# Kernel tuning notes

Measured on AMD Instinct MI355X. Metric: run time of the kernel, lower is better.

Reference implementation:

```python
import jax, jax.numpy as jnp
import numpy as np

EPS = 1e-6

def setup_inputs() -> dict:
    key = jax.random.key(0)
    k1, k2, k3 = jax.random.split(key, 3)
    N, L, S, H, D = 8, 4096, 4096, 8, 64
    queries = jax.random.normal(k1, (N, L, H, D), dtype=jnp.float32)
    keys = jax.random.normal(k2, (N, S, H, D), dtype=jnp.float32)
    values = jax.random.normal(k3, (N, S, H, D), dtype=jnp.float32)
    return {"queries": queries, "keys": keys, "values": values}

def reference(queries, keys, values):
    # elu(x)+1 feature maps (positive kernel)
    Q = jax.nn.elu(queries) + 1.0  # [N,L,H,D]
    K = jax.nn.elu(keys) + 1.0     # [N,S,H,D]
    v_length = values.shape[1]
    v = values / v_length          # scale for numerical stability
    # per-head KV state: [N,H,D,Dv]
    KV = jnp.einsum('nshd,nshv->nhdv', K, v)
    # normalizer: [N,L,H]
    K_sum = K.sum(axis=1)  # [N,H,D]
    Z = 1.0 / (jnp.einsum('nlhd,nhd->nlh', Q, K_sum) + EPS)
    out = jnp.einsum('nlhd,nhdv,nlh->nlhv', Q, KV, Z) * v_length
    return out
```

## Files before the change

### kernel.cpp

```cpp
#include <hip/hip_runtime.h>
#include <hip/hip_bf16.h>
#include <cstddef>
#include <cstdint>

#define N_B   8
#define L_L   4096
#define S_S   4096
#define H_H   8
#define D_D   64
#define NH    64
#define KVLD  68
#define KVSZ  (65 * KVLD)

typedef const float __attribute__((address_space(1)))* gas_fp;
typedef float __attribute__((address_space(3)))* las_fp;

__device__ __forceinline__ float elu1(float x) {
    return x > 0.f ? x + 1.f : __expf(x);
}

__global__ __launch_bounds__(256, 3)
void la_phase1(const float* __restrict__ Kin, const float* __restrict__ Vin,
               float* __restrict__ partials, int split, int schunk)
{
    __shared__ union {
        struct { float K[64 * 64]; float V[2][64 * 64]; } st;
        float acc[64 * 68];
    } sm;
    __shared__ float sKsumP[4 * 64];

    const int b     = blockIdx.x;
    const int nh    = b / split;
    const int chunk = b - nh * split;
    const int n     = nh >> 3;
    const int h     = nh & 7;
    const int s0    = chunk * schunk;

    const int tid  = threadIdx.x;
    const int w    = tid >> 6;
    const int lane = tid & 63;
    const int dg   = lane >> 3;
    const int vg   = lane & 7;

    float acc[8][8];
    #pragma unroll
    for (int i = 0; i < 8; ++i)
        #pragma unroll
        for (int j = 0; j < 8; ++j) acc[i][j] = 0.f;
    float ksum = 0.f;

    const int kd = lane;

    const int lrow = lane >> 4;
    const int lcol = (lane & 15) * 4;

    const float* Kb = Kin + (size_t)n * S_S * (H_H * D_D) + h * D_D;
    const float* Vb = Vin + (size_t)n * S_S * (H_H * D_D) + h * D_D;

    const int ntiles = schunk >> 6;

    #pragma unroll
    for (int c = 0; c < 4; ++c) {
        const int r = w * 16 + c * 4 + lrow;
        __builtin_amdgcn_global_load_lds(
            (gas_fp)(Vb + (size_t)(s0 + r) * (H_H * D_D) + lcol),
            (las_fp)&sm.st.V[0][(w * 16 + c * 4) * 64], 16, 0, 0);
    }

    for (int t = 0; t < ntiles; ++t) {
        const int srow = s0 + t * 64;

        #pragma unroll
        for (int c = 0; c < 4; ++c) {
            const int r = w * 16 + c * 4 + lrow;
            float4 kv = *(const float4*)(Kb + (size_t)(srow + r) * (H_H * D_D) + lcol);
            kv.x = elu1(kv.x); kv.y = elu1(kv.y);
            kv.z = elu1(kv.z); kv.w = elu1(kv.w);
            *(float4*)&sm.st.K[(w * 16 + c * 4) * 64 + lane * 4] = kv;
        }

        if (t + 1 < ntiles) {
            const int srn = srow + 64;
            #pragma unroll
            for (int c = 0; c < 4; ++c) {
                const int r = w * 16 + c * 4 + lrow;
                __builtin_amdgcn_global_load_lds(
                    (gas_fp)(Vb + (size_t)(srn + r) * (H_H * D_D) + lcol),
                    (las_fp)&sm.st.V[(t & 1) ^ 1][(w * 16 + c * 4) * 64], 16, 0, 0);
            }
            asm volatile("s_waitcnt vmcnt(4)" ::: "memory");
        } else {
            asm volatile("s_waitcnt vmcnt(0)" ::: "memory");
        }

        const float* Kbuf = sm.st.K;
        const float* Vbuf = sm.st.V[t & 1];

        #pragma unroll 4
        for (int sl = 0; sl < 16; ++sl) {
            const int s = w * 16 + sl;
            const float4 k0 = *(const float4*)&Kbuf[s * 64 + dg * 8];
            const float4 k1 = *(const float4*)&Kbuf[s * 64 + dg * 8 + 4];
            const float4 v0 = *(const float4*)&Vbuf[s * 64 + vg * 8];
            const float4 v1 = *(const float4*)&Vbuf[s * 64 + vg * 8 + 4];
            const float kf[8] = {k0.x, k0.y, k0.z, k0.w, k1.x, k1.y, k1.z, k1.w};
            const float vf[8] = {v0.x, v0.y, v0.z, v0.w, v1.x, v1.y, v1.z, v1.w};
            #pragma unroll
            for (int i = 0; i < 8; ++i)
                #pragma unroll
                for (int j = 0; j < 8; ++j)
                    acc[i][j] = fmaf(kf[i], vf[j], acc[i][j]);
        }
        #pragma unroll
        for (int sl = 0; sl < 16; ++sl)
            ksum += Kbuf[(w * 16 + sl) * 64 + kd];
    }
    __syncthreads();

    for (int ww = 0; ww < 4; ++ww) {
        if (w == ww) {
            #pragma unroll
            for (int i = 0; i < 8; ++i) {
                float* p = &sm.acc[(dg * 8 + i) * 68 + vg * 8];
                if (ww == 0) {
                    *(float4*)p       = make_float4(acc[i][0], acc[i][1], acc[i][2], acc[i][3]);
                    *(float4*)(p + 4) = make_float4(acc[i][4], acc[i][5], acc[i][6], acc[i][7]);
                } else {
                    float4 a0 = *(const float4*)p;
                    float4 a1 = *(const float4*)(p + 4);
                    a0.x += acc[i][0]; a0.y += acc[i][1]; a0.z += acc[i][2]; a0.w += acc[i][3];
                    a1.x += acc[i][4]; a1.y += acc[i][5]; a1.z += acc[i][6]; a1.w += acc[i][7];
                    *(float4*)p       = a0;
                    *(float4*)(p + 4) = a1;
                }
            }
        }
        __syncthreads();
    }

    sKsumP[w * 64 + kd] = ksum;
    __syncthreads();

    float* outp = partials + (size_t)b * KVSZ;
    for (int idx = tid; idx < KVSZ; idx += 256) {
        const int r = idx / KVLD;
        const int c = idx - r * KVLD;
        float val = 0.f;
        if (c < 64) {
            if (r < 64)
                val = sm.acc[idx];
            else
                val = sKsumP[c] + sKsumP[64 + c] + sKsumP[128 + c] + sKsumP[192 + c];
        }
        outp[idx] = val;
    }
}

__global__ __launch_bounds__(256)
void la_reduce(const float* __restrict__ partials, float* __restrict__ kvt, int split)
{
    const int idx = blockIdx.x * 256 + threadIdx.x;
    if (idx >= NH * KVSZ) return;
    const int nh  = idx / KVSZ;
    const int rem = idx - nh * KVSZ;
    const float* p = partials + (size_t)nh * split * KVSZ + rem;
    float s = 0.f;
    for (int c = 0; c < split; ++c) s += p[(size_t)c * KVSZ];
    kvt[idx] = s;
}

__global__ __launch_bounds__(256, 2)
void la_phase2(const float* __restrict__ Qin, const float* __restrict__ kvt,
               float* __restrict__ Out)
{
    __shared__ float sQ[128 * 68];
    __shared__ float sKV[KVSZ];

    const int b   = blockIdx.x;
    const int nh  = b >> 5;
    const int lc  = b & 31;
    const int n   = nh >> 3;
    const int h   = nh & 7;
    const int tid = threadIdx.x;
    const int w    = tid >> 6;
    const int lane = tid & 63;

    const float* Qc = Qin + (((size_t)n * L_L + (size_t)lc * 128) * H_H + h) * D_D;
    float*       Oc = Out + (((size_t)n * L_L + (size_t)lc * 128) * H_H + h) * D_D;

    {
        const float4* src = (const float4*)(kvt + (size_t)nh * KVSZ);
        float4*       dst = (float4*)sKV;
        #pragma unroll
        for (int it = 0; it < 4; ++it)
            dst[it * 256 + tid] = src[it * 256 + tid];
        if (tid < 81) dst[1024 + tid] = src[1024 + tid];
    }

    #pragma unroll
    for (int it = 0; it < 8; ++it) {
        const int slot = it * 256 + tid;
        const int r    = slot >> 4;
        const int c4   = slot & 15;
        float4 v = *(const float4*)(Qc + (size_t)r * (H_H * D_D) + c4 * 4);
        v.x = elu1(v.x); v.y = elu1(v.y); v.z = elu1(v.z); v.w = elu1(v.w);
        *(float4*)&sQ[r * 68 + c4 * 4] = v;
    }
    __syncthreads();

    const int rt   = (w >> 1) * 64;
    const int wc   = w & 1;
    const int rl   = lane & 7;
    const int cg   = lane >> 3;
    const int ccol = wc * 32 + cg * 4;

    float acc[8][4];
    float den[8];
    #pragma unroll
    for (int j = 0; j < 8; ++j) {
        den[j] = 0.f;
        #pragma unroll
        for (int m = 0; m < 4; ++m) acc[j][m] = 0.f;
    }

    const int qbase = rt + rl;

    for (int kc = 0; kc < 16; ++kc) {
        float4 qv[8];
        #pragma unroll
        for (int j = 0; j < 8; ++j)
            qv[j] = *(const float4*)&sQ[(qbase + 8 * j) * 68 + kc * 4];
        const float4 kv0 = *(const float4*)&sKV[(kc * 4 + 0) * KVLD + ccol];
        const float4 kv1 = *(const float4*)&sKV[(kc * 4 + 1) * KVLD + ccol];
        const float4 kv2 = *(const float4*)&sKV[(kc * 4 + 2) * KVLD + ccol];
        const float4 kv3 = *(const float4*)&sKV[(kc * 4 + 3) * KVLD + ccol];
        const float4 ks  = *(const float4*)&sKV[64 * KVLD + kc * 4];

        #pragma unroll
        for (int j = 0; j < 8; ++j) {
            const float q0 = qv[j].x, q1 = qv[j].y, q2 = qv[j].z, q3 = qv[j].w;
            den[j] = fmaf(q0, ks.x, den[j]);
            den[j] = fmaf(q1, ks.y, den[j]);
            den[j] = fmaf(q2, ks.z, den[j]);
            den[j] = fmaf(q3, ks.w, den[j]);
            acc[j][0] = fmaf(q0, kv0.x, acc[j][0]);
            acc[j][0] = fmaf(q1, kv1.x, acc[j][0]);
            acc[j][0] = fmaf(q2, kv2.x, acc[j][0]);
            acc[j][0] = fmaf(q3, kv3.x, acc[j][0]);
            acc[j][1] = fmaf(q0, kv0.y, acc[j][1]);
            acc[j][1] = fmaf(q1, kv1.y, acc[j][1]);
            acc[j][1] = fmaf(q2, kv2.y, acc[j][1]);
            acc[j][1] = fmaf(q3, kv3.y, acc[j][1]);
            acc[j][2] = fmaf(q0, kv0.z, acc[j][2]);
            acc[j][2] = fmaf(q1, kv1.z, acc[j][2]);
            acc[j][2] = fmaf(q2, kv2.z, acc[j][2]);
            acc[j][2] = fmaf(q3, kv3.z, acc[j][2]);
            acc[j][3] = fmaf(q0, kv0.w, acc[j][3]);
            acc[j][3] = fmaf(q1, kv1.w, acc[j][3]);
            acc[j][3] = fmaf(q2, kv2.w, acc[j][3]);
            acc[j][3] = fmaf(q3, kv3.w, acc[j][3]);
        }
    }

    #pragma unroll
    for (int j = 0; j < 8; ++j) {
        const float rz = 1.0f / (den[j] + 1e-6f);
        *(float4*)(Oc + (size_t)(qbase + 8 * j) * (H_H * D_D) + ccol) =
            make_float4(acc[j][0] * rz, acc[j][1] * rz,
                        acc[j][2] * rz, acc[j][3] * rz);
    }
}

extern "C" void kernel_launch(void* const* d_in, const int* in_sizes, int n_in,
                              void* d_out, int out_size, void* d_ws, size_t ws_size,
                              hipStream_t stream)
{
    const float* Q = (const float*)d_in[0];
    const float* K = (const float*)d_in[1];
    const float* V = (const float*)d_in[2];
    float* out = (float*)d_out;

    float* kvt = (float*)d_ws;
    const size_t kvt_bytes = (size_t)NH * KVSZ * sizeof(float);

    int split = 16;
    while (split > 1 &&
           kvt_bytes + (size_t)NH * split * KVSZ * sizeof(float) > ws_size)
        split >>= 1;
    float* partials = kvt + (size_t)NH * KVSZ;
    const int schunk = S_S / split;

    la_phase1<<<NH * split, 256, 0, stream>>>(K, V, partials, split, schunk);

    const int red_blocks = (NH * KVSZ + 255) / 256;
    la_reduce<<<red_blocks, 256, 0, stream>>>(partials, kvt, split);

    la_phase2<<<NH * (L_L / 128), 256, 0, stream>>>(Q, kvt, out);
}
```

Before: 98.74 us.

## Software-pipeline K loads into registers during phase-1 compute, halve split

Phase 1 now issues the next tile's K global loads into registers, along with the V global-to-LDS loads, before computing on the current tile. It applies ELU and writes K to shared memory only after the compute finishes, so K load latency overlaps the FMA work. Scheduling barriers keep the compiler from moving the loads past the compute. Launch bounds drop to 2 waves per SIMD, allowing more registers for the in-flight K data, and the S split falls from 16 to 8, giving fewer blocks with longer loops and less partial-reduction work. The single K buffer is overwritten right after compute without a barrier, which relies on each wave reading only its own rows; fewer blocks and lower occupancy may reduce parallelism.

```diff
diff --git a/kernel.cpp b/kernel.cpp
--- a/kernel.cpp
+++ b/kernel.cpp
@@ -19,7 +19,7 @@
     return x > 0.f ? x + 1.f : __expf(x);
 }
 
-__global__ __launch_bounds__(256, 3)
+__global__ __launch_bounds__(256, 2)
 void la_phase1(const float* __restrict__ Kin, const float* __restrict__ Vin,
                float* __restrict__ partials, int split, int schunk)
 {
@@ -59,62 +59,84 @@
 
     const int ntiles = schunk >> 6;
 
-    #pragma unroll
-    for (int c = 0; c < 4; ++c) {
-        const int r = w * 16 + c * 4 + lrow;
-        __builtin_amdgcn_global_load_lds(
-            (gas_fp)(Vb + (size_t)(s0 + r) * (H_H * D_D) + lcol),
-            (las_fp)&sm.st.V[0][(w * 16 + c * 4) * 64], 16, 0, 0);
+    float4 ka0, ka1, ka2, ka3;
+
+#define ELU4(X) do { X.x = elu1(X.x); X.y = elu1(X.y); \
+                     X.z = elu1(X.z); X.w = elu1(X.w); } while (0)
+
+    {
+        #pragma unroll
+        for (int c = 0; c < 4; ++c) {
+            __builtin_amdgcn_global_load_lds(
+                (gas_fp)(Vb + (size_t)(s0 + w * 16 + c * 4 + lrow) * (H_H * D_D) + lcol),
+                (las_fp)&sm.st.V[0][(w * 16 + c * 4) * 64], 16, 0, 0);
+        }
+        ka0 = *(const float4*)(Kb + (size_t)(s0 + w * 16 +  0 + lrow) * (H_H * D_D) + lcol);
+        ka1 = *(const float4*)(Kb + (size_t)(s0 + w * 16 +  4 + lrow) * (H_H * D_D) + lcol);
+        ka2 = *(const float4*)(Kb + (size_t)(s0 + w * 16 +  8 + lrow) * (H_H * D_D) + lcol);
+        ka3 = *(const float4*)(Kb + (size_t)(s0 + w * 16 + 12 + lrow) * (H_H * D_D) + lcol);
+        asm volatile("s_waitcnt vmcnt(0)" ::: "memory");
+        ELU4(ka0); ELU4(ka1); ELU4(ka2); ELU4(ka3);
+        *(float4*)&sm.st.K[(w * 16 +  0) * 64 + lane * 4] = ka0;
+        *(float4*)&sm.st.K[(w * 16 +  4) * 64 + lane * 4] = ka1;
+        *(float4*)&sm.st.K[(w * 16 +  8) * 64 + lane * 4] = ka2;
+        *(float4*)&sm.st.K[(w * 16 + 12) * 64 + lane * 4] = ka3;
     }
 
     for (int t = 0; t < ntiles; ++t) {
-        const int srow = s0 + t * 64;
-
-        #pragma unroll
-        for (int c = 0; c < 4; ++c) {
-            const int r = w * 16 + c * 4 + lrow;
-            float4 kv = *(const float4*)(Kb + (size_t)(srow + r) * (H_H * D_D) + lcol);
-            kv.x = elu1(kv.x); kv.y = elu1(kv.y);
-            kv.z = elu1(kv.z); kv.w = elu1(kv.w);
-            *(float4*)&sm.st.K[(w * 16 + c * 4) * 64 + lane * 4] = kv;
-        }
-
-        if (t + 1 < ntiles) {
-            const int srn = srow + 64;
+        const bool more = (t + 1 < ntiles);
+
+        if (more) {
+            const int srn = s0 + (t + 1) * 64;
+            float* vdst = sm.st.V[(t + 1) & 1];
             #pragma unroll
             for (int c = 0; c < 4; ++c) {
-                const int r = w * 16 + c * 4 + lrow;
                 __builtin_amdgcn_global_load_lds(
-                    (gas_fp)(Vb + (size_t)(srn + r) * (H_H * D_D) + lcol),
-                    (las_fp)&sm.st.V[(t & 1) ^ 1][(w * 16 + c * 4) * 64], 16, 0, 0);
+                    (gas_fp)(Vb + (size_t)(srn + w * 16 + c * 4 + lrow) * (H_H * D_D) + lcol),
+                    (las_fp)&vdst[(w * 16 + c * 4) * 64], 16, 0, 0);
             }
-            asm volatile("s_waitcnt vmcnt(4)" ::: "memory");
-        } else {
+            ka0 = *(const float4*)(Kb + (size_t)(srn + w * 16 +  0 + lrow) * (H_H * D_D) + lcol);
+            ka1 = *(const float4*)(Kb + (size_t)(srn + w * 16 +  4 + lrow) * (H_H * D_D) + lcol);
+            ka2 = *(const float4*)(Kb + (size_t)(srn + w * 16 +  8 + lrow) * (H_H * D_D) + lcol);
+            ka3 = *(const float4*)(Kb + (size_t)(srn + w * 16 + 12 + lrow) * (H_H * D_D) + lcol);
+        }
+        __builtin_amdgcn_sched_barrier(0);
+
+        {
+            const float* Kbuf = sm.st.K;
+            const float* Vbuf = sm.st.V[t & 1];
+            #pragma unroll 4
+            for (int sl = 0; sl < 16; ++sl) {
+                const int s = w * 16 + sl;
+                const float4 k0 = *(const float4*)&Kbuf[s * 64 + dg * 8];
+                const float4 k1 = *(const float4*)&Kbuf[s * 64 + dg * 8 + 4];
+                const float4 v0 = *(const float4*)&Vbuf[s * 64 + vg * 8];
+                const float4 v1 = *(const float4*)&Vbuf[s * 64 + vg * 8 + 4];
+                const float kf[8] = {k0.x, k0.y, k0.z, k0.w, k1.x, k1.y, k1.z, k1.w};
+                const float vf[8] = {v0.x, v0.y, v0.z, v0.w, v1.x, v1.y, v1.z, v1.w};
+                #pragma unroll
+                for (int i = 0; i < 8; ++i)
+                    #pragma unroll
+                    for (int j = 0; j < 8; ++j)
+                        acc[i][j] = fmaf(kf[i], vf[j], acc[i][j]);
+            }
+            #pragma unroll
+            for (int sl = 0; sl < 16; ++sl)
+                ksum += Kbuf[(w * 16 + sl) * 64 + kd];
+        }
+        __builtin_amdgcn_sched_barrier(0);
+
+        if (more) {
             asm volatile("s_waitcnt vmcnt(0)" ::: "memory");
-        }
-
-        const float* Kbuf = sm.st.K;
-        const float* Vbuf = sm.st.V[t & 1];
-
-        #pragma unroll 4
-        for (int sl = 0; sl < 16; ++sl) {
-            const int s = w * 16 + sl;
-            const float4 k0 = *(const float4*)&Kbuf[s * 64 + dg * 8];
-            const float4 k1 = *(const float4*)&Kbuf[s * 64 + dg * 8 + 4];
-            const float4 v0 = *(const float4*)&Vbuf[s * 64 + vg * 8];
-            const float4 v1 = *(const float4*)&Vbuf[s * 64 + vg * 8 + 4];
-            const float kf[8] = {k0.x, k0.y, k0.z, k0.w, k1.x, k1.y, k1.z, k1.w};
-            const float vf[8] = {v0.x, v0.y, v0.z, v0.w, v1.x, v1.y, v1.z, v1.w};
-            #pragma unroll
-            for (int i = 0; i < 8; ++i)
-                #pragma unroll
-                for (int j = 0; j < 8; ++j)
-                    acc[i][j] = fmaf(kf[i], vf[j], acc[i][j]);
-        }
-        #pragma unroll
-        for (int sl = 0; sl < 16; ++sl)
-            ksum += Kbuf[(w * 16 + sl) * 64 + kd];
-    }
+            ELU4(ka0); ELU4(ka1); ELU4(ka2); ELU4(ka3);
+            *(float4*)&sm.st.K[(w * 16 +  0) * 64 + lane * 4] = ka0;
+            *(float4*)&sm.st.K[(w * 16 +  4) * 64 + lane * 4] = ka1;
+            *(float4*)&sm.st.K[(w * 16 +  8) * 64 + lane * 4] = ka2;
+            *(float4*)&sm.st.K[(w * 16 + 12) * 64 + lane * 4] = ka3;
+        }
+    }
+#undef ELU4
+
     __syncthreads();
 
     for (int ww = 0; ww < 4; ++ww) {
@@ -283,7 +305,7 @@
     float* kvt = (float*)d_ws;
     const size_t kvt_bytes = (size_t)NH * KVSZ * sizeof(float);
 
-    int split = 16;
+    int split = 8;
     while (split > 1 &&
            kvt_bytes + (size_t)NH * split * KVSZ * sizeof(float) > ws_size)
         split >>= 1;
```

Measured after the change: 90.62 us. 8.2% less time.
